# Kernel optimization log

Measured on AMD Instinct MI355X. Metric: run time of the kernel, lower is better.

Reference implementation:

```python
import jax, jax.numpy as jnp
import numpy as np

N_ACT = 3  # [relu, tanh, sigmoid]


def setup_inputs() -> dict:
    key = jax.random.key(0)
    k1, k2, k3 = jax.random.split(key, 3)
    B, IN, OUT = 4096, 4096, 4096
    x = jax.random.normal(k1, (B, IN), dtype=jnp.float32)
    W = jax.random.normal(k2, (OUT, IN), dtype=jnp.float32)
    b = jax.random.normal(k3, (OUT,), dtype=jnp.float32)
    return {"x": x, "W": W, "b": b}


def reference(x, W, b):
    # Linear: y = x @ W^T + b  -> [B, OUT]
    y = jnp.einsum("bi,oi->bo", x, W) + b
    # Per-output-column criterion: mean over batch, then idx = int(mean % 3).
    # torch `%` on tensors is remainder with the divisor's sign (non-negative
    # here), and int() then truncates == floor for non-negative values.
    means = jnp.mean(y, axis=0)                        # [OUT]
    idx = jnp.mod(means, float(N_ACT)).astype(jnp.int32)  # [OUT] in {0,1,2}
    idx_b = idx[None, :]                               # broadcast over batch
    # Device-side branchless select among the three activations.
    out = jnp.where(
        idx_b == 0,
        jax.nn.relu(y),
        jnp.where(idx_b == 1, jnp.tanh(y), jax.nn.sigmoid(y)),
    )
    return out
```

## Files before the change

kernel.cpp:

```cpp
#include <hip/hip_runtime.h>
#include <hip/hip_bf16.h>
#include <math.h>

#define B_DIM   4096
#define IN_DIM  4096
#define OUT_DIM 4096

typedef __attribute__((ext_vector_type(8))) short  short8;
typedef __attribute__((ext_vector_type(4))) float  floatx4;

__device__ __forceinline__ ushort f2bf(float f) {
    unsigned b = __float_as_uint(f);
    return (ushort)((b + 0x7fffu + ((b >> 16) & 1u)) >> 16);
}

__global__ void cvt_x_colsum(const float* __restrict__ x, ushort* __restrict__ xb,
                             double* __restrict__ part) {
    int c0 = blockIdx.x * 1024 + threadIdx.x * 4;
    int r0 = blockIdx.y * 16;
    double s0 = 0, s1 = 0, s2 = 0, s3 = 0;
#pragma unroll 4
    for (int r = 0; r < 16; ++r) {
        size_t off = (size_t)(r0 + r) * IN_DIM + c0;
        float4 v = *(const float4*)(x + off);
        ushort4 o;
        o.x = f2bf(v.x); o.y = f2bf(v.y); o.z = f2bf(v.z); o.w = f2bf(v.w);
        *(ushort4*)(xb + off) = o;
        s0 += (double)v.x; s1 += (double)v.y; s2 += (double)v.z; s3 += (double)v.w;
    }
    double* p = part + (size_t)blockIdx.y * IN_DIM + c0;
    p[0] = s0; p[1] = s1; p[2] = s2; p[3] = s3;
}

__global__ void xbar_reduce(const double* __restrict__ part, double* __restrict__ xbar) {
    __shared__ double red[256];
    int col   = blockIdx.x * 64 + (threadIdx.x & 63);
    int slice = threadIdx.x >> 6;
    double s = 0.0;
    for (int rb = slice * 64; rb < slice * 64 + 64; ++rb)
        s += part[(size_t)rb * IN_DIM + col];
    red[threadIdx.x] = s;
    __syncthreads();
    if (slice == 0) {
        double v = red[threadIdx.x] + red[threadIdx.x + 64]
                 + red[threadIdx.x + 128] + red[threadIdx.x + 192];
        xbar[col] = v * (1.0 / (double)B_DIM);
    }
}

__global__ void cvt_w_means(const float* __restrict__ W, const float* __restrict__ bias,
                            const double* __restrict__ xbar, ushort* __restrict__ wb,
                            int* __restrict__ idx) {
    __shared__ double red[256];
    int o = blockIdx.x;
    size_t base = (size_t)o * IN_DIM;
    double s = 0.0;
#pragma unroll
    for (int j = 0; j < 4; ++j) {
        int i = j * 1024 + threadIdx.x * 4;
        float4 v = *(const float4*)(W + base + i);
        ushort4 ob;
        ob.x = f2bf(v.x); ob.y = f2bf(v.y); ob.z = f2bf(v.z); ob.w = f2bf(v.w);
        *(ushort4*)(wb + base + i) = ob;
        double2 xv0 = *(const double2*)(xbar + i);
        double2 xv1 = *(const double2*)(xbar + i + 2);
        s += (double)v.x * xv0.x + (double)v.y * xv0.y
           + (double)v.z * xv1.x + (double)v.w * xv1.y;
    }
    red[threadIdx.x] = s;
    __syncthreads();
    for (int st = 128; st > 0; st >>= 1) {
        if (threadIdx.x < st) red[threadIdx.x] += red[threadIdx.x + st];
        __syncthreads();
    }
    if (threadIdx.x == 0) {
        float mf = (float)(red[0] + (double)bias[o]);
        float md = fmodf(mf, 3.0f);
        if (md < 0.0f) md += 3.0f;
        idx[o] = (int)md;
    }
}

__global__ void __launch_bounds__(512, 2) gemm_bt_act(
    const ushort* __restrict__ A,
    const ushort* __restrict__ Bt,
    const float*  __restrict__ bias,
    const int*    __restrict__ idx,
    float*        __restrict__ out) {
    __shared__ __align__(16) ushort lds[4][2][256 * 32];

    const int t    = threadIdx.x;
    const int w    = t >> 6;
    const int l    = t & 63;
    const int quad = l >> 4;
    const int lrow = l & 15;
    const int wm   = w >> 2;
    const int wn   = w & 3;

    const int b   = blockIdx.x;
    const int xcd = b & 7;
    const int p   = b >> 3;
    const int m0  = ((xcd >> 1) * 4 + (p >> 3)) * 256;
    const int n0  = ((xcd & 1) * 8 + (p & 7)) * 256;

    const int K = IN_DIM;

    size_t aoff[2], boff[2];
    int    ldso[2];
#pragma unroll
    for (int j = 0; j < 2; ++j) {
        int chunk = j * 512 + t;
        int r     = chunk >> 2;
        int kb    = (chunk & 3) ^ ((r >> 1) & 3);
        aoff[j] = (size_t)(m0 + r) * K + kb * 8;
        boff[j] = (size_t)(n0 + r) * K + kb * 8;
        ldso[j] = chunk * 8;
    }

    const int kbsw  = (quad ^ ((lrow >> 1) & 3)) * 16;
    const int abase = (wm * 128 + lrow) * 64 + kbsw;
    const int bbase = (wn * 64 + lrow) * 64 + kbsw;

    floatx4 acc[8][4] = {};

#pragma unroll
    for (int pt = 0; pt < 3; ++pt) {
        int ks = pt * 32;
#pragma unroll
        for (int j = 0; j < 2; ++j) {
            __builtin_amdgcn_global_load_lds(
                (__attribute__((address_space(1))) void*)(A + aoff[j] + ks),
                (__attribute__((address_space(3))) void*)(&lds[pt][0][ldso[j]]), 16, 0, 0);
            __builtin_amdgcn_global_load_lds(
                (__attribute__((address_space(1))) void*)(Bt + boff[j] + ks),
                (__attribute__((address_space(3))) void*)(&lds[pt][1][ldso[j]]), 16, 0, 0);
        }
    }

#pragma unroll 1
    for (int kt = 0; kt < 128; ++kt) {
        asm volatile("s_waitcnt vmcnt(8)" ::: "memory");
        __builtin_amdgcn_s_barrier();

        {
            int nt   = (kt + 3) & 127;
            int slot = (kt + 3) & 3;
            int ks   = nt * 32;
#pragma unroll
            for (int j = 0; j < 2; ++j) {
                __builtin_amdgcn_global_load_lds(
                    (__attribute__((address_space(1))) void*)(A + aoff[j] + ks),
                    (__attribute__((address_space(3))) void*)(&lds[slot][0][ldso[j]]), 16, 0, 0);
                __builtin_amdgcn_global_load_lds(
                    (__attribute__((address_space(1))) void*)(Bt + boff[j] + ks),
                    (__attribute__((address_space(3))) void*)(&lds[slot][1][ldso[j]]), 16, 0, 0);
            }
        }

        const char* sa = (const char*)&lds[kt & 3][0][0];
        const char* sb = (const char*)&lds[kt & 3][1][0];
        short8 af[8], bf[4];
#pragma unroll
        for (int mi = 0; mi < 8; ++mi)
            af[mi] = *(const short8*)(sa + abase + mi * 1024);
#pragma unroll
        for (int ni = 0; ni < 4; ++ni)
            bf[ni] = *(const short8*)(sb + bbase + ni * 1024);

        __builtin_amdgcn_s_setprio(1);
#pragma unroll
        for (int mi = 0; mi < 8; ++mi)
#pragma unroll
            for (int ni = 0; ni < 4; ++ni)
                acc[mi][ni] = __builtin_amdgcn_mfma_f32_16x16x32_bf16(
                    af[mi], bf[ni], acc[mi][ni], 0, 0, 0);
        __builtin_amdgcn_s_setprio(0);
    }

#pragma unroll
    for (int ni = 0; ni < 4; ++ni) {
        int   col     = n0 + wn * 64 + ni * 16 + lrow;
        int   id      = idx[col];
        float bv      = bias[col];
        float a       = (id == 1) ? -2.0f : -1.0f;
        bool  isrelu  = (id == 0);
        bool  istanh  = (id == 1);
#pragma unroll
        for (int mi = 0; mi < 8; ++mi) {
            int rowb = m0 + wm * 128 + mi * 16 + quad * 4;
#pragma unroll
            for (int r = 0; r < 4; ++r) {
                float y   = acc[mi][ni][r] + bv;
                float e   = __expf(a * y);
                float s   = __builtin_amdgcn_rcpf(1.0f + e);
                float act = istanh ? fmaf(2.0f, s, -1.0f) : s;
                float v   = isrelu ? fmaxf(y, 0.0f) : act;
                out[(size_t)(rowb + r) * OUT_DIM + col] = v;
            }
        }
    }
}

extern "C" void kernel_launch(void* const* d_in, const int* in_sizes, int n_in,
                              void* d_out, int out_size, void* d_ws, size_t ws_size,
                              hipStream_t stream) {
    const float* x = (const float*)d_in[0];
    const float* W = (const float*)d_in[1];
    const float* b = (const float*)d_in[2];
    float* out = (float*)d_out;

    char* ws = (char*)d_ws;
    ushort* xb   = (ushort*)(ws);
    ushort* wb   = (ushort*)(ws + (33554432));
    double* part = (double*)(ws + (67108864));
    double* xbar = (double*)(ws + (67108864 + 8388608));
    int*    idx  = (int*)   (ws + (67108864 + 8388608 + 32768));

    cvt_x_colsum<<<dim3(4, 256), 256, 0, stream>>>(x, xb, part);
    xbar_reduce<<<64, 256, 0, stream>>>(part, xbar);
    cvt_w_means<<<4096, 256, 0, stream>>>(W, b, xbar, wb, idx);
    gemm_bt_act<<<256, 512, 0, stream>>>(xb, wb, b, idx, out);
}
```

Measured before the change: 322.4 us.

## Split GEMM k-step into two MFMA phases, atomic column sums, shuffle reduction

The GEMM main loop is split into two halves. Each half issues part of the LDS fragment reads and part of the next tile's global-to-LDS loads (A in the first half, B in the second), with barriers in between, so memory traffic interleaves with MFMA work. Separately, the partial column-sum buffer and its reduce kernel are replaced by double atomicAdds into a zeroed xbar, and the block reduction in the W-means kernel now uses wave shuffles. The atomics make the summation order nondeterministic, which could flip an activation index whose mean sits near a boundary, and the extra barriers per k-step add synchronisation cost.

```diff
diff --git a/kernel.cpp b/kernel.cpp
--- a/kernel.cpp
+++ b/kernel.cpp
@@ -15,7 +15,7 @@
 }
 
 __global__ void cvt_x_colsum(const float* __restrict__ x, ushort* __restrict__ xb,
-                             double* __restrict__ part) {
+                             double* __restrict__ xbar_sum) {
     int c0 = blockIdx.x * 1024 + threadIdx.x * 4;
     int r0 = blockIdx.y * 16;
     double s0 = 0, s1 = 0, s2 = 0, s3 = 0;
@@ -28,30 +28,15 @@
         *(ushort4*)(xb + off) = o;
         s0 += (double)v.x; s1 += (double)v.y; s2 += (double)v.z; s3 += (double)v.w;
     }
-    double* p = part + (size_t)blockIdx.y * IN_DIM + c0;
-    p[0] = s0; p[1] = s1; p[2] = s2; p[3] = s3;
-}
-
-__global__ void xbar_reduce(const double* __restrict__ part, double* __restrict__ xbar) {
-    __shared__ double red[256];
-    int col   = blockIdx.x * 64 + (threadIdx.x & 63);
-    int slice = threadIdx.x >> 6;
-    double s = 0.0;
-    for (int rb = slice * 64; rb < slice * 64 + 64; ++rb)
-        s += part[(size_t)rb * IN_DIM + col];
-    red[threadIdx.x] = s;
-    __syncthreads();
-    if (slice == 0) {
-        double v = red[threadIdx.x] + red[threadIdx.x + 64]
-                 + red[threadIdx.x + 128] + red[threadIdx.x + 192];
-        xbar[col] = v * (1.0 / (double)B_DIM);
-    }
+    double* p = xbar_sum + c0;
+    atomicAdd(p + 0, s0); atomicAdd(p + 1, s1);
+    atomicAdd(p + 2, s2); atomicAdd(p + 3, s3);
 }
 
 __global__ void cvt_w_means(const float* __restrict__ W, const float* __restrict__ bias,
-                            const double* __restrict__ xbar, ushort* __restrict__ wb,
+                            const double* __restrict__ xbar_sum, ushort* __restrict__ wb,
                             int* __restrict__ idx) {
-    __shared__ double red[256];
+    __shared__ double red4[4];
     int o = blockIdx.x;
     size_t base = (size_t)o * IN_DIM;
     double s = 0.0;
@@ -62,19 +47,18 @@
         ushort4 ob;
         ob.x = f2bf(v.x); ob.y = f2bf(v.y); ob.z = f2bf(v.z); ob.w = f2bf(v.w);
         *(ushort4*)(wb + base + i) = ob;
-        double2 xv0 = *(const double2*)(xbar + i);
-        double2 xv1 = *(const double2*)(xbar + i + 2);
+        double2 xv0 = *(const double2*)(xbar_sum + i);
+        double2 xv1 = *(const double2*)(xbar_sum + i + 2);
         s += (double)v.x * xv0.x + (double)v.y * xv0.y
            + (double)v.z * xv1.x + (double)v.w * xv1.y;
     }
-    red[threadIdx.x] = s;
+#pragma unroll
+    for (int off = 32; off; off >>= 1) s += __shfl_down(s, off, 64);
+    if ((threadIdx.x & 63) == 0) red4[threadIdx.x >> 6] = s;
     __syncthreads();
-    for (int st = 128; st > 0; st >>= 1) {
-        if (threadIdx.x < st) red[threadIdx.x] += red[threadIdx.x + st];
-        __syncthreads();
-    }
     if (threadIdx.x == 0) {
-        float mf = (float)(red[0] + (double)bias[o]);
+        double tot = red4[0] + red4[1] + red4[2] + red4[3];
+        float mf = (float)(tot * (1.0 / (double)B_DIM) + (double)bias[o]);
         float md = fmodf(mf, 3.0f);
         if (md < 0.0f) md += 3.0f;
         idx[o] = (int)md;
@@ -136,45 +120,62 @@
                 (__attribute__((address_space(3))) void*)(&lds[pt][1][ldso[j]]), 16, 0, 0);
         }
     }
+    asm volatile("s_waitcnt vmcnt(8)" ::: "memory");
+    __builtin_amdgcn_s_barrier();
 
 #pragma unroll 1
     for (int kt = 0; kt < 128; ++kt) {
-        asm volatile("s_waitcnt vmcnt(8)" ::: "memory");
-        __builtin_amdgcn_s_barrier();
-
-        {
-            int nt   = (kt + 3) & 127;
-            int slot = (kt + 3) & 3;
-            int ks   = nt * 32;
-#pragma unroll
-            for (int j = 0; j < 2; ++j) {
-                __builtin_amdgcn_global_load_lds(
-                    (__attribute__((address_space(1))) void*)(A + aoff[j] + ks),
-                    (__attribute__((address_space(3))) void*)(&lds[slot][0][ldso[j]]), 16, 0, 0);
-                __builtin_amdgcn_global_load_lds(
-                    (__attribute__((address_space(1))) void*)(Bt + boff[j] + ks),
-                    (__attribute__((address_space(3))) void*)(&lds[slot][1][ldso[j]]), 16, 0, 0);
-            }
-        }
-
         const char* sa = (const char*)&lds[kt & 3][0][0];
         const char* sb = (const char*)&lds[kt & 3][1][0];
+        const int nt   = (kt + 3) & 127;
+        const int slot = (kt + 3) & 3;
+        const int ks   = nt * 32;
+
         short8 af[8], bf[4];
-#pragma unroll
-        for (int mi = 0; mi < 8; ++mi)
+
+#pragma unroll
+        for (int mi = 0; mi < 4; ++mi)
             af[mi] = *(const short8*)(sa + abase + mi * 1024);
 #pragma unroll
         for (int ni = 0; ni < 4; ++ni)
             bf[ni] = *(const short8*)(sb + bbase + ni * 1024);
-
+#pragma unroll
+        for (int j = 0; j < 2; ++j)
+            __builtin_amdgcn_global_load_lds(
+                (__attribute__((address_space(1))) void*)(A + aoff[j] + ks),
+                (__attribute__((address_space(3))) void*)(&lds[slot][0][ldso[j]]), 16, 0, 0);
+
+        __builtin_amdgcn_s_barrier();
         __builtin_amdgcn_s_setprio(1);
 #pragma unroll
-        for (int mi = 0; mi < 8; ++mi)
+        for (int mi = 0; mi < 4; ++mi)
 #pragma unroll
             for (int ni = 0; ni < 4; ++ni)
                 acc[mi][ni] = __builtin_amdgcn_mfma_f32_16x16x32_bf16(
                     af[mi], bf[ni], acc[mi][ni], 0, 0, 0);
         __builtin_amdgcn_s_setprio(0);
+        __builtin_amdgcn_s_barrier();
+
+#pragma unroll
+        for (int mi = 4; mi < 8; ++mi)
+            af[mi] = *(const short8*)(sa + abase + mi * 1024);
+#pragma unroll
+        for (int j = 0; j < 2; ++j)
+            __builtin_amdgcn_global_load_lds(
+                (__attribute__((address_space(1))) void*)(Bt + boff[j] + ks),
+                (__attribute__((address_space(3))) void*)(&lds[slot][1][ldso[j]]), 16, 0, 0);
+
+        asm volatile("s_waitcnt vmcnt(8)" ::: "memory");
+        __builtin_amdgcn_s_barrier();
+        __builtin_amdgcn_s_setprio(1);
+#pragma unroll
+        for (int mi = 4; mi < 8; ++mi)
+#pragma unroll
+            for (int ni = 0; ni < 4; ++ni)
+                acc[mi][ni] = __builtin_amdgcn_mfma_f32_16x16x32_bf16(
+                    af[mi], bf[ni], acc[mi][ni], 0, 0, 0);
+        __builtin_amdgcn_s_setprio(0);
+        __builtin_amdgcn_s_barrier();
     }
 
 #pragma unroll
@@ -211,13 +212,12 @@
 
     char* ws = (char*)d_ws;
     ushort* xb   = (ushort*)(ws);
-    ushort* wb   = (ushort*)(ws + (33554432));
-    double* part = (double*)(ws + (67108864));
-    double* xbar = (double*)(ws + (67108864 + 8388608));
-    int*    idx  = (int*)   (ws + (67108864 + 8388608 + 32768));
-
-    cvt_x_colsum<<<dim3(4, 256), 256, 0, stream>>>(x, xb, part);
-    xbar_reduce<<<64, 256, 0, stream>>>(part, xbar);
+    ushort* wb   = (ushort*)(ws + 33554432);
+    double* xbar = (double*)(ws + 67108864);
+    int*    idx  = (int*)   (ws + 67108864 + 32768);
+
+    hipMemsetAsync(xbar, 0, IN_DIM * sizeof(double), stream);
+    cvt_x_colsum<<<dim3(4, 256), 256, 0, stream>>>(x, xb, xbar);
     cvt_w_means<<<4096, 256, 0, stream>>>(W, b, xbar, wb, idx);
     gemm_bt_act<<<256, 512, 0, stream>>>(xb, wb, b, idx, out);
 }
```

After: 310.6 us. -3.6%, faster.
